# Performance work log

Hardware: AMD Instinct MI355X
Metric: run time of the kernel (lower is better)

The kernel has to match this reference:

```python
import jax, jax.numpy as jnp
import numpy as np

B = 262144
C = 195  # number of countries
EARTH_R = 6371.0  # km


def setup_inputs() -> dict:
    key = jax.random.key(0)
    k1, k2, k3, k4 = jax.random.split(key, 4)
    logits = jax.random.normal(k1, (B, C), dtype=jnp.float32)
    target = jax.random.randint(k2, (B,), 0, C)
    # country coordinates: lat in [-90, 90], lon in [-180, 180]
    lat = jax.random.uniform(k3, (C,), minval=-90.0, maxval=90.0, dtype=jnp.float32)
    lon = jax.random.uniform(k4, (C,), minval=-180.0, maxval=180.0, dtype=jnp.float32)
    coords = jnp.stack([lat, lon], axis=-1)  # [C, 2]
    return {"logits": logits, "target": target, "coords": coords}


def _haversine(lat1, lon1, lat2, lon2):
    lat1, lon1, lat2, lon2 = map(jnp.deg2rad, (lat1, lon1, lat2, lon2))
    dlat = lat2 - lat1
    dlon = lon2 - lon1
    a = jnp.sin(dlat / 2) ** 2 + jnp.cos(lat1) * jnp.cos(lat2) * jnp.sin(dlon / 2) ** 2
    return 2.0 * EARTH_R * jnp.arcsin(jnp.sqrt(a))


def reference(logits, target, coords):
    # cross entropy (mean reduction)
    logp = jax.nn.log_softmax(logits, axis=-1)  # [B, C]
    ce_loss = -jnp.take_along_axis(logp, target[:, None], axis=1).mean()
    # geographical loss: haversine between argmax-pred country and true country
    preds = jnp.argmax(logits, axis=1)  # [B]
    pc = coords[preds]   # [B, 2]
    tc = coords[target]  # [B, 2]
    dist = _haversine(pc[:, 0], pc[:, 1], tc[:, 0], tc[:, 1])  # [B]
    geo_loss = dist.mean() / 500.0
    return ce_loss + geo_loss
```

## Files before the change

kernel.cpp:

```cpp
#include <hip/hip_runtime.h>
#include <hip/hip_bf16.h>
#include <math.h>

#define NC 195
#define ROWS_PER_BLOCK 16
#define F4_PER_BLOCK (ROWS_PER_BLOCK * NC / 4)

__device__ __forceinline__ float hav_scaled(float lat1, float lon1, float lat2, float lon2) {
    const float d2r = 0.017453292519943295f;
    lat1 *= d2r; lon1 *= d2r; lat2 *= d2r; lon2 *= d2r;
    float sdlat = sinf(0.5f * (lat2 - lat1));
    float sdlon = sinf(0.5f * (lon2 - lon1));
    float a = sdlat * sdlat + cosf(lat1) * cosf(lat2) * sdlon * sdlon;
    a = fminf(fmaxf(a, 0.0f), 1.0f);
    return (2.0f * 6371.0f / 500.0f) * asinf(sqrtf(a));
}

__global__ void dist_kernel(const float* __restrict__ coords, float* __restrict__ distm) {
    int idx = blockIdx.x * 256 + threadIdx.x;
    if (idx >= NC * NC) return;
    int i = idx / NC;
    int j = idx - i * NC;
    distm[idx] = hav_scaled(coords[2 * i], coords[2 * i + 1],
                            coords[2 * j], coords[2 * j + 1]);
}

__global__ __launch_bounds__(256) void main_kernel(const float4* __restrict__ logits4,
                                                   const int* __restrict__ target,
                                                   const float* __restrict__ distm,
                                                   float* __restrict__ partials) {
    __shared__ float lds[ROWS_PER_BLOCK * NC];
    __shared__ float wpart[ROWS_PER_BLOCK];
    const int t = threadIdx.x;
    const long long base4 = (long long)blockIdx.x * F4_PER_BLOCK;
    float4* lds4 = (float4*)lds;

    lds4[t]       = logits4[base4 + t];
    lds4[t + 256] = logits4[base4 + t + 256];
    lds4[t + 512] = logits4[base4 + t + 512];
    if (t < F4_PER_BLOCK - 768) lds4[t + 768] = logits4[base4 + t + 768];
    __syncthreads();

    const int lane = t & 63;
    const int u = lane & 15;
    const int r = t >> 4;
    const float* __restrict__ rowp = lds + r * NC;

    float x[13];
    #pragma unroll
    for (int k = 0; k < 12; ++k) x[k] = rowp[u + 16 * k];
    x[12] = (u < NC - 192) ? rowp[u + 192] : -INFINITY;

    float m = x[0]; int mi = u;
    #pragma unroll
    for (int k = 1; k < 13; ++k) {
        if (x[k] > m) { m = x[k]; mi = u + 16 * k; }
    }

    #pragma unroll
    for (int off = 8; off > 0; off >>= 1) {
        float om = __shfl_xor(m, off);
        int   oi = __shfl_xor(mi, off);
        if (om > m || (om == m && oi < mi)) { m = om; mi = oi; }
    }

    float s = 0.0f;
    #pragma unroll
    for (int k = 0; k < 13; ++k) s += __expf(x[k] - m);
    #pragma unroll
    for (int off = 8; off > 0; off >>= 1) s += __shfl_xor(s, off);

    if (u == 0) {
        long long row = (long long)blockIdx.x * ROWS_PER_BLOCK + r;
        int tg = target[row];
        float ce = (m + __logf(s)) - rowp[tg];
        wpart[r] = ce + distm[mi * NC + tg];
    }
    __syncthreads();
    if (t == 0) {
        float v = 0.0f;
        #pragma unroll
        for (int i = 0; i < ROWS_PER_BLOCK; ++i) v += wpart[i];
        partials[blockIdx.x] = v;
    }
}

__global__ __launch_bounds__(1024) void reduce_kernel(const float* __restrict__ partials,
                                                      int n, float inv_b,
                                                      float* __restrict__ out) {
    float s = 0.0f;
    for (int i = threadIdx.x; i < n; i += 1024) s += partials[i];
    #pragma unroll
    for (int off = 32; off > 0; off >>= 1) s += __shfl_xor(s, off);
    __shared__ float ws[16];
    const int wave = threadIdx.x >> 6;
    const int lane = threadIdx.x & 63;
    if (lane == 0) ws[wave] = s;
    __syncthreads();
    if (threadIdx.x == 0) {
        float tot = 0.0f;
        #pragma unroll
        for (int w = 0; w < 16; ++w) tot += ws[w];
        out[0] = tot * inv_b;
    }
}

extern "C" void kernel_launch(void* const* d_in, const int* in_sizes, int n_in,
                              void* d_out, int out_size, void* d_ws, size_t ws_size,
                              hipStream_t stream) {
    const float* logits = (const float*)d_in[0];
    const int*   target = (const int*)d_in[1];
    const float* coords = (const float*)d_in[2];
    float* out = (float*)d_out;

    const int B = in_sizes[1];
    const int n_blocks = B / ROWS_PER_BLOCK;

    float* partials = (float*)d_ws;
    float* distm = partials + n_blocks;

    dist_kernel<<<(NC * NC + 255) / 256, 256, 0, stream>>>(coords, distm);
    main_kernel<<<n_blocks, 256, 0, stream>>>((const float4*)logits, target, distm, partials);
    reduce_kernel<<<1, 1024, 0, stream>>>(partials, n_blocks, 1.0f / (float)B, out);
}
```

Measured before the change: 49.01 us.

## Split final reduction into two kernels and stage targets in LDS

Replaces the single-block 1024-thread reduction over 16384 partials with a two-stage reduction: 64 blocks of 256 each produce one partial, then a 64-thread kernel sums those. This spreads the final reduction across many CUs instead of one block looping serially. The targets for each block are now loaded cooperatively into LDS before the sync instead of by one lane per row afterward. It adds one more kernel launch and hardcodes the assumption that n_blocks is exactly 64*256.

```diff
diff --git a/kernel.cpp b/kernel.cpp
--- a/kernel.cpp
+++ b/kernel.cpp
@@ -30,6 +30,7 @@
                                                    const float* __restrict__ distm,
                                                    float* __restrict__ partials) {
     __shared__ float lds[ROWS_PER_BLOCK * NC];
+    __shared__ int tgt[ROWS_PER_BLOCK];
     __shared__ float wpart[ROWS_PER_BLOCK];
     const int t = threadIdx.x;
     const long long base4 = (long long)blockIdx.x * F4_PER_BLOCK;
@@ -39,6 +40,7 @@
     lds4[t + 256] = logits4[base4 + t + 256];
     lds4[t + 512] = logits4[base4 + t + 512];
     if (t < F4_PER_BLOCK - 768) lds4[t + 768] = logits4[base4 + t + 768];
+    if (t < ROWS_PER_BLOCK) tgt[t] = target[(long long)blockIdx.x * ROWS_PER_BLOCK + t];
     __syncthreads();
 
     const int lane = t & 63;
@@ -71,8 +73,7 @@
     for (int off = 8; off > 0; off >>= 1) s += __shfl_xor(s, off);
 
     if (u == 0) {
-        long long row = (long long)blockIdx.x * ROWS_PER_BLOCK + r;
-        int tg = target[row];
+        int tg = tgt[r];
         float ce = (m + __logf(s)) - rowp[tg];
         wpart[r] = ce + distm[mi * NC + tg];
     }
@@ -85,24 +86,23 @@
     }
 }
 
-__global__ __launch_bounds__(1024) void reduce_kernel(const float* __restrict__ partials,
-                                                      int n, float inv_b,
-                                                      float* __restrict__ out) {
-    float s = 0.0f;
-    for (int i = threadIdx.x; i < n; i += 1024) s += partials[i];
+__global__ __launch_bounds__(256) void reduce1_kernel(const float* __restrict__ partials,
+                                                      float* __restrict__ stage2) {
+    float s = partials[blockIdx.x * 256 + threadIdx.x];
     #pragma unroll
     for (int off = 32; off > 0; off >>= 1) s += __shfl_xor(s, off);
-    __shared__ float ws[16];
-    const int wave = threadIdx.x >> 6;
-    const int lane = threadIdx.x & 63;
-    if (lane == 0) ws[wave] = s;
+    __shared__ float ws[4];
+    if ((threadIdx.x & 63) == 0) ws[threadIdx.x >> 6] = s;
     __syncthreads();
-    if (threadIdx.x == 0) {
-        float tot = 0.0f;
-        #pragma unroll
-        for (int w = 0; w < 16; ++w) tot += ws[w];
-        out[0] = tot * inv_b;
-    }
+    if (threadIdx.x == 0) stage2[blockIdx.x] = ws[0] + ws[1] + ws[2] + ws[3];
+}
+
+__global__ void reduce2_kernel(const float* __restrict__ stage2, float inv_b,
+                               float* __restrict__ out) {
+    float s = stage2[threadIdx.x];
+    #pragma unroll
+    for (int off = 32; off > 0; off >>= 1) s += __shfl_xor(s, off);
+    if (threadIdx.x == 0) out[0] = s * inv_b;
 }
 
 extern "C" void kernel_launch(void* const* d_in, const int* in_sizes, int n_in,
@@ -117,9 +117,11 @@
     const int n_blocks = B / ROWS_PER_BLOCK;
 
     float* partials = (float*)d_ws;
-    float* distm = partials + n_blocks;
+    float* stage2 = partials + n_blocks;
+    float* distm = stage2 + 64;
 
     dist_kernel<<<(NC * NC + 255) / 256, 256, 0, stream>>>(coords, distm);
     main_kernel<<<n_blocks, 256, 0, stream>>>((const float4*)logits, target, distm, partials);
-    reduce_kernel<<<1, 1024, 0, stream>>>(partials, n_blocks, 1.0f / (float)B, out);
+    reduce1_kernel<<<n_blocks / 256, 256, 0, stream>>>(partials, stage2);
+    reduce2_kernel<<<1, 64, 0, stream>>>(stage2, 1.0f / (float)B, out);
 }
```

New measurement: 46.12 us. 5.9% less time.

## Process eight row chunks per block with register-prefetched double buffering

Applied to the files above, without the earlier changes.

Each block now walks 8 chunks of 16 rows. It loads the next chunk's logits into registers while computing on the current chunk held in LDS, and targets are staged once per block. This cuts the block count eightfold and overlaps global loads with compute, which shrinks the partials array so the final reduce reads exactly two values per thread. The reduce now hardcodes 2048 partials, which holds only for this B, and fewer blocks may reduce latency hiding across CUs.

```diff
diff --git a/kernel.cpp b/kernel.cpp
--- a/kernel.cpp
+++ b/kernel.cpp
@@ -3,8 +3,10 @@
 #include <math.h>
 
 #define NC 195
-#define ROWS_PER_BLOCK 16
-#define F4_PER_BLOCK (ROWS_PER_BLOCK * NC / 4)
+#define ROWS_PER_CHUNK 16
+#define CHUNKS_PER_BLOCK 8
+#define BLOCK_ROWS (ROWS_PER_CHUNK * CHUNKS_PER_BLOCK)
+#define F4_PER_CHUNK (ROWS_PER_CHUNK * NC / 4)
 
 __device__ __forceinline__ float hav_scaled(float lat1, float lon1, float lat2, float lon2) {
     const float d2r = 0.017453292519943295f;
@@ -29,73 +31,93 @@
                                                    const int* __restrict__ target,
                                                    const float* __restrict__ distm,
                                                    float* __restrict__ partials) {
-    __shared__ float lds[ROWS_PER_BLOCK * NC];
-    __shared__ float wpart[ROWS_PER_BLOCK];
+    __shared__ float lds[ROWS_PER_CHUNK * NC];
+    __shared__ int tgt[BLOCK_ROWS];
+    __shared__ float wpart[16];
     const int t = threadIdx.x;
-    const long long base4 = (long long)blockIdx.x * F4_PER_BLOCK;
     float4* lds4 = (float4*)lds;
 
-    lds4[t]       = logits4[base4 + t];
-    lds4[t + 256] = logits4[base4 + t + 256];
-    lds4[t + 512] = logits4[base4 + t + 512];
-    if (t < F4_PER_BLOCK - 768) lds4[t + 768] = logits4[base4 + t + 768];
+    const long long row0 = (long long)blockIdx.x * BLOCK_ROWS;
+    if (t < BLOCK_ROWS) tgt[t] = target[row0 + t];
+
+    const long long base4 = (long long)blockIdx.x * CHUNKS_PER_BLOCK * F4_PER_CHUNK;
+
+    float4 n0 = logits4[base4 + t];
+    float4 n1 = logits4[base4 + t + 256];
+    float4 n2 = logits4[base4 + t + 512];
+    float4 n3;
+    if (t < F4_PER_CHUNK - 768) n3 = logits4[base4 + t + 768];
+    lds4[t] = n0; lds4[t + 256] = n1; lds4[t + 512] = n2;
+    if (t < F4_PER_CHUNK - 768) lds4[t + 768] = n3;
     __syncthreads();
 
-    const int lane = t & 63;
-    const int u = lane & 15;
+    const int u = t & 15;
     const int r = t >> 4;
     const float* __restrict__ rowp = lds + r * NC;
+    float acc = 0.0f;
 
-    float x[13];
-    #pragma unroll
-    for (int k = 0; k < 12; ++k) x[k] = rowp[u + 16 * k];
-    x[12] = (u < NC - 192) ? rowp[u + 192] : -INFINITY;
+    for (int i = 0; i < CHUNKS_PER_BLOCK; ++i) {
+        const bool has_next = (i + 1 < CHUNKS_PER_BLOCK);
+        if (has_next) {
+            const long long nb = base4 + (long long)(i + 1) * F4_PER_CHUNK;
+            n0 = logits4[nb + t];
+            n1 = logits4[nb + t + 256];
+            n2 = logits4[nb + t + 512];
+            if (t < F4_PER_CHUNK - 768) n3 = logits4[nb + t + 768];
+        }
 
-    float m = x[0]; int mi = u;
-    #pragma unroll
-    for (int k = 1; k < 13; ++k) {
-        if (x[k] > m) { m = x[k]; mi = u + 16 * k; }
+        float x[13];
+        #pragma unroll
+        for (int k = 0; k < 12; ++k) x[k] = rowp[u + 16 * k];
+        x[12] = (u < NC - 192) ? rowp[u + 192] : -INFINITY;
+
+        float m = x[0]; int mi = u;
+        #pragma unroll
+        for (int k = 1; k < 13; ++k) {
+            if (x[k] > m) { m = x[k]; mi = u + 16 * k; }
+        }
+        #pragma unroll
+        for (int off = 8; off > 0; off >>= 1) {
+            float om = __shfl_xor(m, off);
+            int   oi = __shfl_xor(mi, off);
+            if (om > m || (om == m && oi < mi)) { m = om; mi = oi; }
+        }
+        float s = 0.0f;
+        #pragma unroll
+        for (int k = 0; k < 13; ++k) s += __expf(x[k] - m);
+        #pragma unroll
+        for (int off = 8; off > 0; off >>= 1) s += __shfl_xor(s, off);
+
+        if (u == 0) {
+            int tg = tgt[i * ROWS_PER_CHUNK + r];
+            float ce = (m + __logf(s)) - rowp[tg];
+            acc += ce + distm[mi * NC + tg];
+        }
+        __syncthreads();
+        if (has_next) {
+            lds4[t] = n0; lds4[t + 256] = n1; lds4[t + 512] = n2;
+            if (t < F4_PER_CHUNK - 768) lds4[t + 768] = n3;
+            __syncthreads();
+        }
     }
 
-    #pragma unroll
-    for (int off = 8; off > 0; off >>= 1) {
-        float om = __shfl_xor(m, off);
-        int   oi = __shfl_xor(mi, off);
-        if (om > m || (om == m && oi < mi)) { m = om; mi = oi; }
-    }
-
-    float s = 0.0f;
-    #pragma unroll
-    for (int k = 0; k < 13; ++k) s += __expf(x[k] - m);
-    #pragma unroll
-    for (int off = 8; off > 0; off >>= 1) s += __shfl_xor(s, off);
-
-    if (u == 0) {
-        long long row = (long long)blockIdx.x * ROWS_PER_BLOCK + r;
-        int tg = target[row];
-        float ce = (m + __logf(s)) - rowp[tg];
-        wpart[r] = ce + distm[mi * NC + tg];
-    }
+    if (u == 0) wpart[r] = acc;
     __syncthreads();
     if (t == 0) {
         float v = 0.0f;
         #pragma unroll
-        for (int i = 0; i < ROWS_PER_BLOCK; ++i) v += wpart[i];
+        for (int j = 0; j < 16; ++j) v += wpart[j];
         partials[blockIdx.x] = v;
     }
 }
 
 __global__ __launch_bounds__(1024) void reduce_kernel(const float* __restrict__ partials,
-                                                      int n, float inv_b,
-                                                      float* __restrict__ out) {
-    float s = 0.0f;
-    for (int i = threadIdx.x; i < n; i += 1024) s += partials[i];
+                                                      float inv_b, float* __restrict__ out) {
+    float s = partials[threadIdx.x] + partials[threadIdx.x + 1024];
     #pragma unroll
     for (int off = 32; off > 0; off >>= 1) s += __shfl_xor(s, off);
     __shared__ float ws[16];
-    const int wave = threadIdx.x >> 6;
-    const int lane = threadIdx.x & 63;
-    if (lane == 0) ws[wave] = s;
+    if ((threadIdx.x & 63) == 0) ws[threadIdx.x >> 6] = s;
     __syncthreads();
     if (threadIdx.x == 0) {
         float tot = 0.0f;
@@ -114,12 +136,12 @@
     float* out = (float*)d_out;
 
     const int B = in_sizes[1];
-    const int n_blocks = B / ROWS_PER_BLOCK;
+    const int n_blocks = B / BLOCK_ROWS;
 
     float* partials = (float*)d_ws;
     float* distm = partials + n_blocks;
 
     dist_kernel<<<(NC * NC + 255) / 256, 256, 0, stream>>>(coords, distm);
     main_kernel<<<n_blocks, 256, 0, stream>>>((const float4*)logits, target, distm, partials);
-    reduce_kernel<<<1, 1024, 0, stream>>>(partials, n_blocks, 1.0f / (float)B, out);
+    reduce_kernel<<<1, 1024, 0, stream>>>(partials, 1.0f / (float)B, out);
 }
```

After: 45.59 us. 7.0% less time.

## Read logits directly per wave, loop rows, fuse final reduction via last-block atomic

Applied to the files above, without the earlier changes.

Drops the LDS staging of logits. Each wave now loops over 32 rows, reading them straight from global memory, so each block covers 128 rows instead of 16. The separate reduce kernel is replaced by a last-block-done pattern: an atomic counter, reset in the distance kernel, lets the final block sum the partials. This saves a kernel launch and the LDS traffic, but the global loads become strided per row (uncoalesced 16-lane segments), and the final reduction hardcodes exactly 2048 partials.

```diff
diff --git a/kernel.cpp b/kernel.cpp
--- a/kernel.cpp
+++ b/kernel.cpp
@@ -3,8 +3,9 @@
 #include <math.h>
 
 #define NC 195
-#define ROWS_PER_BLOCK 16
-#define F4_PER_BLOCK (ROWS_PER_BLOCK * NC / 4)
+#define ROWS_PER_BLOCK 128
+#define ROWS_PER_WAVE 32
+#define ITERS 8
 
 __device__ __forceinline__ float hav_scaled(float lat1, float lon1, float lat2, float lon2) {
     const float d2r = 0.017453292519943295f;
@@ -16,7 +17,9 @@
     return (2.0f * 6371.0f / 500.0f) * asinf(sqrtf(a));
 }
 
-__global__ void dist_kernel(const float* __restrict__ coords, float* __restrict__ distm) {
+__global__ void dist_kernel(const float* __restrict__ coords, float* __restrict__ distm,
+                            unsigned int* __restrict__ counter) {
+    if (blockIdx.x == 0 && threadIdx.x == 0) *counter = 0u;
     int idx = blockIdx.x * 256 + threadIdx.x;
     if (idx >= NC * NC) return;
     int i = idx / NC;
@@ -25,83 +28,79 @@
                             coords[2 * j], coords[2 * j + 1]);
 }
 
-__global__ __launch_bounds__(256) void main_kernel(const float4* __restrict__ logits4,
+__global__ __launch_bounds__(256) void main_kernel(const float* __restrict__ logits,
                                                    const int* __restrict__ target,
                                                    const float* __restrict__ distm,
-                                                   float* __restrict__ partials) {
-    __shared__ float lds[ROWS_PER_BLOCK * NC];
-    __shared__ float wpart[ROWS_PER_BLOCK];
+                                                   float* __restrict__ partials,
+                                                   unsigned int* __restrict__ counter,
+                                                   float inv_b,
+                                                   float* __restrict__ out) {
     const int t = threadIdx.x;
-    const long long base4 = (long long)blockIdx.x * F4_PER_BLOCK;
-    float4* lds4 = (float4*)lds;
-
-    lds4[t]       = logits4[base4 + t];
-    lds4[t + 256] = logits4[base4 + t + 256];
-    lds4[t + 512] = logits4[base4 + t + 512];
-    if (t < F4_PER_BLOCK - 768) lds4[t + 768] = logits4[base4 + t + 768];
-    __syncthreads();
-
+    const int wave = t >> 6;
     const int lane = t & 63;
     const int u = lane & 15;
-    const int r = t >> 4;
-    const float* __restrict__ rowp = lds + r * NC;
+    const int r = lane >> 4;
+    const long long wrow0 = (long long)blockIdx.x * ROWS_PER_BLOCK
+                          + (long long)wave * ROWS_PER_WAVE;
+    float acc = 0.0f;
 
-    float x[13];
-    #pragma unroll
-    for (int k = 0; k < 12; ++k) x[k] = rowp[u + 16 * k];
-    x[12] = (u < NC - 192) ? rowp[u + 192] : -INFINITY;
+    for (int i = 0; i < ITERS; ++i) {
+        const long long row = wrow0 + i * 4 + r;
+        const float* __restrict__ rowp = logits + row * NC;
 
-    float m = x[0]; int mi = u;
-    #pragma unroll
-    for (int k = 1; k < 13; ++k) {
-        if (x[k] > m) { m = x[k]; mi = u + 16 * k; }
+        float x[13];
+        #pragma unroll
+        for (int k = 0; k < 12; ++k) x[k] = rowp[u + 16 * k];
+        x[12] = (u < 3) ? rowp[192 + u] : -INFINITY;
+
+        float m = x[0]; int mi = u;
+        #pragma unroll
+        for (int k = 1; k < 13; ++k) {
+            if (x[k] > m) { m = x[k]; mi = u + 16 * k; }
+        }
+        #pragma unroll
+        for (int off = 8; off > 0; off >>= 1) {
+            float om = __shfl_xor(m, off);
+            int   oi = __shfl_xor(mi, off);
+            if (om > m || (om == m && oi < mi)) { m = om; mi = oi; }
+        }
+        float s = 0.0f;
+        #pragma unroll
+        for (int k = 0; k < 13; ++k) s += __expf(x[k] - m);
+        #pragma unroll
+        for (int off = 8; off > 0; off >>= 1) s += __shfl_xor(s, off);
+
+        if (u == 0) {
+            int tg = target[row];
+            float ce = (m + __logf(s)) - rowp[tg];
+            acc += ce + distm[mi * NC + tg];
+        }
     }
 
-    #pragma unroll
-    for (int off = 8; off > 0; off >>= 1) {
-        float om = __shfl_xor(m, off);
-        int   oi = __shfl_xor(mi, off);
-        if (om > m || (om == m && oi < mi)) { m = om; mi = oi; }
-    }
-
-    float s = 0.0f;
-    #pragma unroll
-    for (int k = 0; k < 13; ++k) s += __expf(x[k] - m);
-    #pragma unroll
-    for (int off = 8; off > 0; off >>= 1) s += __shfl_xor(s, off);
-
-    if (u == 0) {
-        long long row = (long long)blockIdx.x * ROWS_PER_BLOCK + r;
-        int tg = target[row];
-        float ce = (m + __logf(s)) - rowp[tg];
-        wpart[r] = ce + distm[mi * NC + tg];
-    }
+    __shared__ float wpart[16];
+    __shared__ bool amLast;
+    if (u == 0) wpart[wave * 4 + r] = acc;
     __syncthreads();
     if (t == 0) {
         float v = 0.0f;
         #pragma unroll
-        for (int i = 0; i < ROWS_PER_BLOCK; ++i) v += wpart[i];
+        for (int j = 0; j < 16; ++j) v += wpart[j];
         partials[blockIdx.x] = v;
+        __threadfence();
+        unsigned int old = atomicAdd(counter, 1u);
+        amLast = (old == gridDim.x - 1);
     }
-}
-
-__global__ __launch_bounds__(1024) void reduce_kernel(const float* __restrict__ partials,
-                                                      int n, float inv_b,
-                                                      float* __restrict__ out) {
-    float s = 0.0f;
-    for (int i = threadIdx.x; i < n; i += 1024) s += partials[i];
-    #pragma unroll
-    for (int off = 32; off > 0; off >>= 1) s += __shfl_xor(s, off);
-    __shared__ float ws[16];
-    const int wave = threadIdx.x >> 6;
-    const int lane = threadIdx.x & 63;
-    if (lane == 0) ws[wave] = s;
     __syncthreads();
-    if (threadIdx.x == 0) {
-        float tot = 0.0f;
+    if (amLast) {
+        __threadfence();
+        float s = 0.0f;
         #pragma unroll
-        for (int w = 0; w < 16; ++w) tot += ws[w];
-        out[0] = tot * inv_b;
+        for (int j = 0; j < 8; ++j) s += partials[t + 256 * j];
+        #pragma unroll
+        for (int off = 32; off > 0; off >>= 1) s += __shfl_xor(s, off);
+        if (lane == 0) wpart[wave] = s;
+        __syncthreads();
+        if (t == 0) out[0] = (wpart[0] + wpart[1] + wpart[2] + wpart[3]) * inv_b;
     }
 }
 
@@ -117,9 +116,10 @@
     const int n_blocks = B / ROWS_PER_BLOCK;
 
     float* partials = (float*)d_ws;
-    float* distm = partials + n_blocks;
+    unsigned int* counter = (unsigned int*)(partials + n_blocks);
+    float* distm = (float*)(partials + n_blocks + 4);
 
-    dist_kernel<<<(NC * NC + 255) / 256, 256, 0, stream>>>(coords, distm);
-    main_kernel<<<n_blocks, 256, 0, stream>>>((const float4*)logits, target, distm, partials);
-    reduce_kernel<<<1, 1024, 0, stream>>>(partials, n_blocks, 1.0f / (float)B, out);
+    dist_kernel<<<(NC * NC + 255) / 256, 256, 0, stream>>>(coords, distm, counter);
+    main_kernel<<<n_blocks, 256, 0, stream>>>(logits, target, distm, partials,
+                                              counter, 1.0f / (float)B, out);
 }
```

New measurement: 98.16 us. 2x slower.
